# Kernel tuning notes

Hardware: AMD Instinct MI355X
Metric: run time of the kernel (lower is better)

The kernel has to match this reference:

```python
import jax, jax.numpy as jnp
import numpy as np

# dims (match init_kwargs)
N = 262144      # num_memory_locations
D = 128         # dim_memory
C = 512         # dim_controller_output
E_IN = 256      # dim_external_input
OUT = 256       # dim_NTM_output
R = 2           # num_read_heads
WH = 1          # num_write_heads
RAD = 1         # shift_radius
S = 2 * RAD + 1 # shift vector length
EPS = 1e-8


def setup_inputs() -> dict:
    key = jax.random.key(0)
    ks = jax.random.split(key, 40)
    f = lambda i, shape, s=0.05: jax.random.normal(ks[i], shape, dtype=jnp.float32) * s
    inp = {
        "external_input": f(0, (E_IN,), 1.0),
        "M": f(1, (N, D), 1.0),                      # memory matrix
        "prev_read": jnp.zeros((R, D), jnp.float32),  # first step: past readings are zeros
        "Wc": f(2, (C, E_IN + R * D)), "bc": f(3, (C,)),
        "Wo": f(4, (OUT, C + R * D)), "bo": f(5, (OUT,)),
        # read heads (stacked over head axis)
        "rWk": f(6, (R, D, C)),  "rbk": f(7, (R, D)),
        "rWb": f(8, (R, C)),     "rbb": f(9, (R,)),
        "rWg": f(10, (R, C)),    "rbg": f(11, (R,)),
        "rWs": f(12, (R, S, C)), "rbs": f(13, (R, S)),
        "rWgm": f(14, (R, C)),   "rbgm": f(15, (R,)),
        "rinit": f(16, (R, N), 1.0),
        # write heads
        "wWk": f(17, (WH, D, C)),  "wbk": f(18, (WH, D)),
        "wWb": f(19, (WH, C)),     "wbb": f(20, (WH,)),
        "wWg": f(21, (WH, C)),     "wbg": f(22, (WH,)),
        "wWs": f(23, (WH, S, C)),  "wbs": f(24, (WH, S)),
        "wWgm": f(25, (WH, C)),    "wbgm": f(26, (WH,)),
        "wWe": f(27, (WH, D, C)),  "wbe": f(28, (WH, D)),
        "wWa": f(29, (WH, D, C)),  "wba": f(30, (WH, D)),
        "winit": f(31, (WH, N), 1.0),
    }
    return inp


def _address(c, M, Mnorm, w_prev, Wk, bk, Wb, bb, Wg, bg, Ws, bs, Wgm, bgm):
    """Standard NTM addressing: content -> interpolate -> circular shift -> sharpen."""
    k = jnp.tanh(Wk @ c + bk)                       # [D] key
    beta = jax.nn.softplus(Wb @ c + bb)             # scalar key strength
    g = jax.nn.sigmoid(Wg @ c + bg)                 # scalar interpolation gate
    s = jax.nn.softmax(Ws @ c + bs)                 # [S] shift distribution
    gamma = 1.0 + jax.nn.softplus(Wgm @ c + bgm)    # scalar sharpening >= 1
    # content addressing: cosine similarity against all N memory rows
    sim = (M @ k) / (Mnorm * jnp.linalg.norm(k) + EPS)   # [N]
    w_c = jax.nn.softmax(beta * sim)
    # interpolation with previous weighting
    w_g = g * w_c + (1.0 - g) * w_prev
    # circular convolution shift (small fixed radius -> unrolled)
    w_t = jnp.zeros_like(w_g)
    for j, sh in enumerate(range(-RAD, RAD + 1)):
        w_t = w_t + s[j] * jnp.roll(w_g, sh)
    # sharpening
    w_p = w_t ** gamma
    return w_p / (w_p.sum() + EPS)


_address_heads = jax.vmap(_address, in_axes=(None, None, None, 0, 0, 0, 0, 0, 0, 0, 0, 0, 0, 0))


def reference(external_input, M, prev_read, Wc, bc, Wo, bo,
              rWk, rbk, rWb, rbb, rWg, rbg, rWs, rbs, rWgm, rbgm, rinit,
              wWk, wbk, wWb, wbb, wWg, wbg, wWs, wbs, wWgm, wbgm,
              wWe, wbe, wWa, wba, winit):
    # controller
    c = Wc @ jnp.concatenate([external_input, prev_read.reshape(-1)]) + bc   # [C]
    Mnorm = jnp.linalg.norm(M, axis=1)                                        # [N]
    # read heads: addressing (initial weighting = softmax of learned logits) then read
    w_prev_r = jax.nn.softmax(rinit, axis=1)
    read_w = _address_heads(c, M, Mnorm, w_prev_r,
                            rWk, rbk, rWb, rbb, rWg, rbg, rWs, rbs, rWgm, rbgm)  # [R, N]
    readings = read_w @ M                                                     # [R, D]
    # write heads: all weightings computed on pre-write memory
    w_prev_w = jax.nn.softmax(winit, axis=1)
    write_w = _address_heads(c, M, Mnorm, w_prev_w,
                             wWk, wbk, wWb, wbb, wWg, wbg, wWs, wbs, wWgm, wbgm)  # [WH, N]
    # sequential erase-then-add writes
    M_new = M
    for i in range(WH):
        e = jax.nn.sigmoid(wWe[i] @ c + wbe[i])   # [D] erase vector
        a = jnp.tanh(wWa[i] @ c + wba[i])          # [D] add vector
        w = write_w[i][:, None]                    # [N, 1]
        M_new = M_new * (1.0 - w * e[None, :]) + w * a[None, :]
    # NTM output
    out = Wo @ jnp.concatenate([c, readings.reshape(-1)]) + bo               # [OUT]
    return out, readings, read_w, write_w, M_new
```

## Files before the change

kernel.cpp:

```cpp
#include <hip/hip_runtime.h>
#include <hip/hip_bf16.h>

#define NN 262144
#define EPS 1e-8f

#define WS_C      0
#define WS_K      512
#define WS_E      896
#define WS_A      1024
#define WS_KNSQ   1152
#define WS_BETA   1155
#define WS_G      1158
#define WS_GAMMA  1161
#define WS_SL     1164
#define WS_ZC     1184
#define WS_SUMP   1190
#define WS_ZCR    1280
#define WS_SUMPR  1792
#define WS_RDACC  2304
#define WS_ZERO_CNT (WS_RDACC + 2048 - WS_KNSQ)
#define WS_T      4608
#define WS_NEEDED ((size_t)(WS_T + 3 * NN) * 4)

#define OUT_OUT   0
#define OUT_READ  256
#define OUT_RW    512
#define OUT_WW    (512 + 2 * NN)
#define OUT_MNEW  ((size_t)(512 + 3 * NN))

__global__ void FFNTM_78477642433000_kernel(int* p) { if (p) *p = 0; }

__device__ __forceinline__ float4 ld4(const float* p) { return *reinterpret_cast<const float4*>(p); }

__device__ __forceinline__ float wred(float v) {
#pragma unroll
    for (int off = 32; off > 0; off >>= 1) v += __shfl_xor(v, off);
    return v;
}

__device__ __forceinline__ void load_shift_params(const float* __restrict__ ws,
        float g[3], float gam[3], float izc[3], float izp[3],
        float s0[3], float s1[3], float s2[3]) {
#pragma unroll
    for (int h = 0; h < 3; h++) {
        g[h]   = ws[WS_G + h];
        gam[h] = ws[WS_GAMMA + h];
        izc[h] = 1.0f / fmaxf(ws[WS_ZC + h],     1e-30f);
        izp[h] = 1.0f / fmaxf(ws[WS_ZC + 3 + h], 1e-30f);
        const float l0 = ws[WS_SL + h*3], l1 = ws[WS_SL + h*3 + 1], l2 = ws[WS_SL + h*3 + 2];
        const float mx = fmaxf(l0, fmaxf(l1, l2));
        const float e0 = expf(l0 - mx), e1 = expf(l1 - mx), e2 = expf(l2 - mx);
        const float inv = 1.0f / (e0 + e1 + e2);
        s0[h] = e0 * inv; s1[h] = e1 * inv; s2[h] = e2 * inv;
    }
}

__global__ void csent(float* out, float val) {
    if (threadIdx.x == 0 && blockIdx.x == 0) out[OUT_OUT] = val;
}

__global__ void __launch_bounds__(256) c0(const float* __restrict__ ei, const float* __restrict__ pr,
                                          const float* __restrict__ Wc, const float* __restrict__ bc,
                                          float* __restrict__ ws) {
    const int t = threadIdx.x;
    const int lane = t & 63;
    const int j = (blockIdx.x * 256 + t) >> 6;

    if (blockIdx.x == 0) {
        for (int i = t; i < WS_ZERO_CNT; i += 256) ws[WS_KNSQ + i] = 0.0f;
    }

    const float* xs = (lane < 32) ? (ei + lane * 8) : (pr + (lane - 32) * 8);
    const float4 xa = ld4(xs), xb = ld4(xs + 4);
    const float* wr = Wc + j * 512 + lane * 8;
    const float4 wa = ld4(wr), wb = ld4(wr + 4);
    float acc = xa.x * wa.x + xa.y * wa.y + xa.z * wa.z + xa.w * wa.w
              + xb.x * wb.x + xb.y * wb.y + xb.z * wb.z + xb.w * wb.w;
    acc = wred(acc);
    if (lane == 0) ws[WS_C + j] = acc + bc[j];
}

__global__ void __launch_bounds__(256) c1(
    const float* __restrict__ rWk, const float* __restrict__ rbk,
    const float* __restrict__ rWb, const float* __restrict__ rbb,
    const float* __restrict__ rWg, const float* __restrict__ rbg,
    const float* __restrict__ rWs, const float* __restrict__ rbs,
    const float* __restrict__ rWgm, const float* __restrict__ rbgm,
    const float* __restrict__ wWk, const float* __restrict__ wbk,
    const float* __restrict__ wWb, const float* __restrict__ wbb,
    const float* __restrict__ wWg, const float* __restrict__ wbg,
    const float* __restrict__ wWs, const float* __restrict__ wbs,
    const float* __restrict__ wWgm, const float* __restrict__ wbgm,
    const float* __restrict__ wWe, const float* __restrict__ wbe,
    const float* __restrict__ wWa, const float* __restrict__ wba,
    float* __restrict__ ws) {
    const int w = blockIdx.x * 4 + (threadIdx.x >> 6);
    const int lane = threadIdx.x & 63;
    if (w >= 658) return;

    const float4 ca = ld4(ws + WS_C + lane * 8);
    const float4 cb = ld4(ws + WS_C + lane * 8 + 4);

    const float* row; float bias; int kind; int h = 0, d = 0, sidx = 0;
    if (w < 384) {
        h = w >> 7; d = w & 127;
        row  = (h < 2) ? (rWk + (h * 128 + d) * 512) : (wWk + d * 512);
        bias = (h < 2) ? rbk[h * 128 + d] : wbk[d];
        kind = 0;
    } else if (w < 512) {
        d = w - 384; row = wWe + d * 512; bias = wbe[d]; kind = 1;
    } else if (w < 640) {
        d = w - 512; row = wWa + d * 512; bias = wba[d]; kind = 2;
    } else if (w < 643) {
        h = w - 640; row = (h < 2) ? (rWb + h * 512) : wWb;
        bias = (h < 2) ? rbb[h] : wbb[0]; kind = 3;
    } else if (w < 646) {
        h = w - 643; row = (h < 2) ? (rWg + h * 512) : wWg;
        bias = (h < 2) ? rbg[h] : wbg[0]; kind = 4;
    } else if (w < 649) {
        h = w - 646; row = (h < 2) ? (rWgm + h * 512) : wWgm;
        bias = (h < 2) ? rbgm[h] : wbgm[0]; kind = 5;
    } else {
        sidx = w - 649; h = sidx / 3; const int jj = sidx % 3;
        row  = (h < 2) ? (rWs + (h * 3 + jj) * 512) : (wWs + jj * 512);
        bias = (h < 2) ? rbs[h * 3 + jj] : wbs[jj];
        kind = 6;
    }

    const float4 ra = ld4(row + lane * 8);
    const float4 rb = ld4(row + lane * 8 + 4);
    float acc = ca.x * ra.x + ca.y * ra.y + ca.z * ra.z + ca.w * ra.w
              + cb.x * rb.x + cb.y * rb.y + cb.z * rb.z + cb.w * rb.w;
    acc = wred(acc);

    if (lane == 0) {
        const float x = acc + bias;
        switch (kind) {
            case 0: { float kv = tanhf(x); ws[WS_K + w] = kv; atomicAdd(&ws[WS_KNSQ + h], kv * kv); } break;
            case 1: ws[WS_E + d] = 1.0f / (1.0f + expf(-x)); break;
            case 2: ws[WS_A + d] = tanhf(x); break;
            case 3: ws[WS_BETA + h] = log1pf(expf(x)); break;
            case 4: ws[WS_G + h] = 1.0f / (1.0f + expf(-x)); break;
            case 5: ws[WS_GAMMA + h] = 1.0f + log1pf(expf(x)); break;
            case 6: ws[WS_SL + sidx] = x; break;
        }
    }
}

__global__ void __launch_bounds__(256) c2(const float* __restrict__ M, const float* __restrict__ rinit,
                                          const float* __restrict__ winit, float* __restrict__ out,
                                          float* __restrict__ ws) {
    const int t = threadIdx.x;
    const int lane = t & 63;
    const int wv = t >> 6;
    const int grp = t >> 5;
    const int sub = lane & 31;

    float kf0[4], kf1[4], kf2[4];
#pragma unroll
    for (int j = 0; j < 4; j++) {
        kf0[j] = ws[WS_K +       sub * 4 + j];
        kf1[j] = ws[WS_K + 128 + sub * 4 + j];
        kf2[j] = ws[WS_K + 256 + sub * 4 + j];
    }
    float beta[3], kn[3];
#pragma unroll
    for (int h = 0; h < 3; h++) { kn[h] = sqrtf(ws[WS_KNSQ + h]); beta[h] = ws[WS_BETA + h]; }

    float zc0 = 0, zc1 = 0, zc2 = 0, zp0 = 0, zp1 = 0, zp2 = 0;

    for (int row = blockIdx.x * 8 + grp; row < NN; row += gridDim.x * 8) {
        const float4 m = ld4(M + (size_t)row * 128 + sub * 4);
        float d0 = m.x * kf0[0] + m.y * kf0[1] + m.z * kf0[2] + m.w * kf0[3];
        float d1 = m.x * kf1[0] + m.y * kf1[1] + m.z * kf1[2] + m.w * kf1[3];
        float d2 = m.x * kf2[0] + m.y * kf2[1] + m.z * kf2[2] + m.w * kf2[3];
        float ns = m.x * m.x + m.y * m.y + m.z * m.z + m.w * m.w;
#pragma unroll
        for (int off = 1; off < 32; off <<= 1) {
            d0 += __shfl_xor(d0, off);
            d1 += __shfl_xor(d1, off);
            d2 += __shfl_xor(d2, off);
            ns += __shfl_xor(ns, off);
        }
        if (sub == 0) {
            const float mn = sqrtf(ns);
            const float t0 = expf(beta[0] * d0 / (mn * kn[0] + EPS));
            const float t1 = expf(beta[1] * d1 / (mn * kn[1] + EPS));
            const float t2 = expf(beta[2] * d2 / (mn * kn[2] + EPS));
            ws[WS_T + row]          = t0;
            ws[WS_T + NN + row]     = t1;
            ws[WS_T + 2 * NN + row] = t2;
            zc0 += t0; zc1 += t1; zc2 += t2;
        }
    }

    float* Esc = out + OUT_MNEW;
    for (int i = blockIdx.x * 256 + t; i < NN; i += gridDim.x * 256) {
        const float e0 = expf(rinit[i]);
        const float e1 = expf(rinit[NN + i]);
        const float e2 = expf(winit[i]);
        Esc[i]          = e0;
        Esc[NN + i]     = e1;
        Esc[2 * NN + i] = e2;
        zp0 += e0; zp1 += e1; zp2 += e2;
    }

    __shared__ float red[4][6];
    float vals[6] = {zc0, zc1, zc2, zp0, zp1, zp2};
#pragma unroll
    for (int q = 0; q < 6; q++) {
        float v = wred(vals[q]);
        if (lane == 0) red[wv][q] = v;
    }
    __syncthreads();
    if (t < 6) {
        atomicAdd(&ws[WS_ZCR + (blockIdx.x & 15) * 32 + t],
                  red[0][t] + red[1][t] + red[2][t] + red[3][t]);
    }
}

__global__ void c2b(float* __restrict__ ws) {
    const int t = threadIdx.x;
    if (t < 6) {
        float s = 0.0f;
#pragma unroll
        for (int r = 0; r < 16; r++) s += ws[WS_ZCR + r * 32 + t];
        ws[WS_ZC + t] = s;
    }
}

__global__ void __launch_bounds__(256) c3(float* __restrict__ out, float* __restrict__ ws) {
    float g[3], gam[3], izc[3], izp[3], s0[3], s1[3], s2[3];
    load_shift_params(ws, g, gam, izc, izp, s0, s1, s2);
    const float* Esc = out + OUT_MNEW;

    float sump[3] = {0.f, 0.f, 0.f};
    for (int i = blockIdx.x * 256 + threadIdx.x; i < NN; i += gridDim.x * 256) {
        const int im = (i == 0) ? (NN - 1) : (i - 1);
        const int ip = (i == NN - 1) ? 0 : (i + 1);
#pragma unroll
        for (int h = 0; h < 3; h++) {
            const float* tp = ws + WS_T + h * NN;
            const float* Ep = Esc + (size_t)h * NN;
            const float gg = g[h], om = 1.0f - gg;
            const float wgm = gg * tp[im] * izc[h] + om * Ep[im] * izp[h];
            const float wg0 = gg * tp[i]  * izc[h] + om * Ep[i]  * izp[h];
            const float wgp = gg * tp[ip] * izc[h] + om * Ep[ip] * izp[h];
            const float wt = fmaxf(s0[h] * wgp + s1[h] * wg0 + s2[h] * wgm, 1e-30f);
            const float p = expf(gam[h] * logf(wt));
            sump[h] += p;
            float* pd = (h == 0) ? (out + OUT_RW) : (h == 1) ? (out + OUT_RW + NN) : (out + OUT_WW);
            pd[i] = p;
        }
    }

    __shared__ float red[4][3];
    const int lane = threadIdx.x & 63, wv = threadIdx.x >> 6;
#pragma unroll
    for (int h = 0; h < 3; h++) {
        float v = wred(sump[h]);
        if (lane == 0) red[wv][h] = v;
    }
    __syncthreads();
    if (threadIdx.x < 3) {
        atomicAdd(&ws[WS_SUMPR + (blockIdx.x & 15) * 32 + threadIdx.x],
                  red[0][threadIdx.x] + red[1][threadIdx.x] + red[2][threadIdx.x] + red[3][threadIdx.x]);
    }
}

__global__ void c3b(float* __restrict__ ws) {
    const int t = threadIdx.x;
    if (t < 3) {
        float s = 0.0f;
#pragma unroll
        for (int r = 0; r < 16; r++) s += ws[WS_SUMPR + r * 32 + t];
        ws[WS_SUMP + t] = s;
    }
}

__global__ void __launch_bounds__(256) c4(const float* __restrict__ M, float* __restrict__ out,
                                          float* __restrict__ ws) {
    float isp[3];
#pragma unroll
    for (int h = 0; h < 3; h++) isp[h] = 1.0f / (ws[WS_SUMP + h] + EPS);

    const int t = threadIdx.x;
    const int lane = t & 63;
    const int wv = t >> 6;
    const int grp = t >> 5;
    const int sub = lane & 31;

    float ev[4], av[4];
#pragma unroll
    for (int j = 0; j < 4; j++) { ev[j] = ws[WS_E + sub * 4 + j]; av[j] = ws[WS_A + sub * 4 + j]; }

    float r0[4] = {0, 0, 0, 0}, r1[4] = {0, 0, 0, 0};

    for (int row = blockIdx.x * 8 + grp; row < NN; row += gridDim.x * 8) {
        const float w0 = out[OUT_RW + row]      * isp[0];
        const float w1 = out[OUT_RW + NN + row] * isp[1];
        const float w2 = out[OUT_WW + row]      * isp[2];
        const float4 m = ld4(M + (size_t)row * 128 + sub * 4);
        float4 nv;
        nv.x = m.x * (1.0f - w2 * ev[0]) + w2 * av[0];
        nv.y = m.y * (1.0f - w2 * ev[1]) + w2 * av[1];
        nv.z = m.z * (1.0f - w2 * ev[2]) + w2 * av[2];
        nv.w = m.w * (1.0f - w2 * ev[3]) + w2 * av[3];
        *reinterpret_cast<float4*>(out + OUT_MNEW + (size_t)row * 128 + sub * 4) = nv;
        r0[0] += w0 * m.x; r0[1] += w0 * m.y; r0[2] += w0 * m.z; r0[3] += w0 * m.w;
        r1[0] += w1 * m.x; r1[1] += w1 * m.y; r1[2] += w1 * m.z; r1[3] += w1 * m.w;
        if (sub == 0) {
            out[OUT_RW + row]      = w0;
            out[OUT_RW + NN + row] = w1;
            out[OUT_WW + row]      = w2;
        }
    }

#pragma unroll
    for (int j = 0; j < 4; j++) {
        r0[j] += __shfl_xor(r0[j], 32);
        r1[j] += __shfl_xor(r1[j], 32);
    }
    __shared__ float lds[4][256];
    if (lane < 32) {
#pragma unroll
        for (int j = 0; j < 4; j++) {
            lds[wv][sub * 4 + j]       = r0[j];
            lds[wv][128 + sub * 4 + j] = r1[j];
        }
    }
    __syncthreads();
    atomicAdd(&ws[WS_RDACC + (blockIdx.x & 7) * 256 + t],
              lds[0][t] + lds[1][t] + lds[2][t] + lds[3][t]);
}

__global__ void __launch_bounds__(256) c5(const float* __restrict__ Wo, const float* __restrict__ bo,
                                          float* __restrict__ ws, float* __restrict__ out) {
    __shared__ float rd[256];
    const int t = threadIdx.x;
    {
        float s = 0.0f;
#pragma unroll
        for (int r = 0; r < 8; r++) s += ws[WS_RDACC + r * 256 + t];
        rd[t] = s;
    }
    __syncthreads();

    const int lane = t & 63;
    const int j = blockIdx.x * 4 + (t >> 6);
    const float* row = Wo + j * 768;
    float acc = 0.0f;
#pragma unroll
    for (int q = 0; q < 12; q++) {
        const int i = lane * 12 + q;
        const float x = (i < 512) ? ws[WS_C + i] : rd[i - 512];
        acc += row[i] * x;
    }
    acc = wred(acc);
    if (lane == 0) out[OUT_OUT + j] = acc + bo[j];
    if (blockIdx.x == 0) out[OUT_READ + t] = rd[t];
}

extern "C" void kernel_launch(void* const* d_in, const int* in_sizes, int n_in,
                              void* d_out, int out_size, void* d_ws, size_t ws_size,
                              hipStream_t stream) {
    float* out = (float*)d_out;

    static const int expect[33] = {
        256, 33554432, 256, 262144, 512, 196608, 256,
        131072, 256, 1024, 2, 1024, 2, 3072, 6, 1024, 2, 524288,
        65536, 128, 512, 1, 512, 1, 1536, 3, 512, 1,
        65536, 128, 65536, 128, 262144
    };
    int bad = (n_in == 33) ? -1 : 33;
    if (bad < 0) {
        for (int i = 0; i < 33; i++) {
            if (in_sizes[i] != expect[i]) { bad = i; break; }
        }
    }
    if (bad >= 0) { csent<<<1, 64, 0, stream>>>(out, 10000.0f + (float)bad); return; }
    if (ws_size < WS_NEEDED) { csent<<<1, 64, 0, stream>>>(out, 5000.0f + (float)(ws_size >> 20)); return; }

    const float* ei    = (const float*)d_in[0];
    const float* M     = (const float*)d_in[1];
    const float* pr    = (const float*)d_in[2];
    const float* Wc    = (const float*)d_in[3];
    const float* bc    = (const float*)d_in[4];
    const float* Wo    = (const float*)d_in[5];
    const float* bo    = (const float*)d_in[6];
    const float* rWk   = (const float*)d_in[7];
    const float* rbk   = (const float*)d_in[8];
    const float* rWb   = (const float*)d_in[9];
    const float* rbb   = (const float*)d_in[10];
    const float* rWg   = (const float*)d_in[11];
    const float* rbg   = (const float*)d_in[12];
    const float* rWs   = (const float*)d_in[13];
    const float* rbs   = (const float*)d_in[14];
    const float* rWgm  = (const float*)d_in[15];
    const float* rbgm  = (const float*)d_in[16];
    const float* rinit = (const float*)d_in[17];
    const float* wWk   = (const float*)d_in[18];
    const float* wbk   = (const float*)d_in[19];
    const float* wWb   = (const float*)d_in[20];
    const float* wbb   = (const float*)d_in[21];
    const float* wWg   = (const float*)d_in[22];
    const float* wbg   = (const float*)d_in[23];
    const float* wWs   = (const float*)d_in[24];
    const float* wbs   = (const float*)d_in[25];
    const float* wWgm  = (const float*)d_in[26];
    const float* wbgm  = (const float*)d_in[27];
    const float* wWe   = (const float*)d_in[28];
    const float* wbe   = (const float*)d_in[29];
    const float* wWa   = (const float*)d_in[30];
    const float* wba   = (const float*)d_in[31];
    const float* winit = (const float*)d_in[32];
    float* ws = (float*)d_ws;

    c0<<<128, 256, 0, stream>>>(ei, pr, Wc, bc, ws);
    c1<<<165, 256, 0, stream>>>(rWk, rbk, rWb, rbb, rWg, rbg, rWs, rbs, rWgm, rbgm,
                                wWk, wbk, wWb, wbb, wWg, wbg, wWs, wbs, wWgm, wbgm,
                                wWe, wbe, wWa, wba, ws);
    c2<<<2048, 256, 0, stream>>>(M, rinit, winit, out, ws);
    c2b<<<1, 64, 0, stream>>>(ws);
    c3<<<1024, 256, 0, stream>>>(out, ws);
    c3b<<<1, 64, 0, stream>>>(ws);
    c4<<<1024, 256, 0, stream>>>(M, out, ws);
    c5<<<64, 256, 0, stream>>>(Wo, bo, ws, out);
}
```

Baseline: 354.7 us.

## Drop tiny partial-sum reduction kernels and widen per-lane row chunks in c2

Removes the single-block c2b and c3b kernels. Each block of c3 and c4 now sums the 16 partial-sum slots itself, which cuts two launches and their serialization gaps. The content-similarity pass in c2 also changes from 32 lanes per row with one float4 each to 8 lanes per row with four float4 each. That shortens the shuffle reduction from five steps to three and puts 32 rows in each block. The trade-off is more registers for the key fragments, redundant tiny reductions in every block, and less coalescing per load instruction.

```diff
diff --git a/kernel.cpp b/kernel.cpp
--- a/kernel.cpp
+++ b/kernel.cpp
@@ -13,8 +13,6 @@
 #define WS_G      1158
 #define WS_GAMMA  1161
 #define WS_SL     1164
-#define WS_ZC     1184
-#define WS_SUMP   1190
 #define WS_ZCR    1280
 #define WS_SUMPR  1792
 #define WS_RDACC  2304
@@ -43,10 +41,16 @@
         float s0[3], float s1[3], float s2[3]) {
 #pragma unroll
     for (int h = 0; h < 3; h++) {
+        float zc = 0.0f, zp = 0.0f;
+#pragma unroll
+        for (int r = 0; r < 16; r++) {
+            zc += ws[WS_ZCR + r * 32 + h];
+            zp += ws[WS_ZCR + r * 32 + 3 + h];
+        }
         g[h]   = ws[WS_G + h];
         gam[h] = ws[WS_GAMMA + h];
-        izc[h] = 1.0f / fmaxf(ws[WS_ZC + h],     1e-30f);
-        izp[h] = 1.0f / fmaxf(ws[WS_ZC + 3 + h], 1e-30f);
+        izc[h] = 1.0f / fmaxf(zc, 1e-30f);
+        izp[h] = 1.0f / fmaxf(zp, 1e-30f);
         const float l0 = ws[WS_SL + h*3], l1 = ws[WS_SL + h*3 + 1], l2 = ws[WS_SL + h*3 + 2];
         const float mx = fmaxf(l0, fmaxf(l1, l2));
         const float e0 = expf(l0 - mx), e1 = expf(l1 - mx), e2 = expf(l2 - mx);
@@ -153,15 +157,15 @@
     const int t = threadIdx.x;
     const int lane = t & 63;
     const int wv = t >> 6;
-    const int grp = t >> 5;
-    const int sub = lane & 31;
-
-    float kf0[4], kf1[4], kf2[4];
-#pragma unroll
-    for (int j = 0; j < 4; j++) {
-        kf0[j] = ws[WS_K +       sub * 4 + j];
-        kf1[j] = ws[WS_K + 128 + sub * 4 + j];
-        kf2[j] = ws[WS_K + 256 + sub * 4 + j];
+    const int rl = lane >> 3;
+    const int cl = lane & 7;
+
+    float kf0[16], kf1[16], kf2[16];
+#pragma unroll
+    for (int j = 0; j < 16; j++) {
+        kf0[j] = ws[WS_K +       cl * 16 + j];
+        kf1[j] = ws[WS_K + 128 + cl * 16 + j];
+        kf2[j] = ws[WS_K + 256 + cl * 16 + j];
     }
     float beta[3], kn[3];
 #pragma unroll
@@ -169,20 +173,25 @@
 
     float zc0 = 0, zc1 = 0, zc2 = 0, zp0 = 0, zp1 = 0, zp2 = 0;
 
-    for (int row = blockIdx.x * 8 + grp; row < NN; row += gridDim.x * 8) {
-        const float4 m = ld4(M + (size_t)row * 128 + sub * 4);
-        float d0 = m.x * kf0[0] + m.y * kf0[1] + m.z * kf0[2] + m.w * kf0[3];
-        float d1 = m.x * kf1[0] + m.y * kf1[1] + m.z * kf1[2] + m.w * kf1[3];
-        float d2 = m.x * kf2[0] + m.y * kf2[1] + m.z * kf2[2] + m.w * kf2[3];
-        float ns = m.x * m.x + m.y * m.y + m.z * m.z + m.w * m.w;
-#pragma unroll
-        for (int off = 1; off < 32; off <<= 1) {
+    for (int row = blockIdx.x * 32 + wv * 8 + rl; row < NN; row += gridDim.x * 32) {
+        const float* mp = M + (size_t)row * 128 + cl * 16;
+        float d0 = 0, d1 = 0, d2 = 0, ns = 0;
+#pragma unroll
+        for (int q = 0; q < 4; q++) {
+            const float4 m = ld4(mp + q * 4);
+            d0 += m.x * kf0[q*4+0] + m.y * kf0[q*4+1] + m.z * kf0[q*4+2] + m.w * kf0[q*4+3];
+            d1 += m.x * kf1[q*4+0] + m.y * kf1[q*4+1] + m.z * kf1[q*4+2] + m.w * kf1[q*4+3];
+            d2 += m.x * kf2[q*4+0] + m.y * kf2[q*4+1] + m.z * kf2[q*4+2] + m.w * kf2[q*4+3];
+            ns += m.x * m.x + m.y * m.y + m.z * m.z + m.w * m.w;
+        }
+#pragma unroll
+        for (int off = 1; off < 8; off <<= 1) {
             d0 += __shfl_xor(d0, off);
             d1 += __shfl_xor(d1, off);
             d2 += __shfl_xor(d2, off);
             ns += __shfl_xor(ns, off);
         }
-        if (sub == 0) {
+        if (cl == 0) {
             const float mn = sqrtf(ns);
             const float t0 = expf(beta[0] * d0 / (mn * kn[0] + EPS));
             const float t1 = expf(beta[1] * d1 / (mn * kn[1] + EPS));
@@ -216,16 +225,6 @@
     if (t < 6) {
         atomicAdd(&ws[WS_ZCR + (blockIdx.x & 15) * 32 + t],
                   red[0][t] + red[1][t] + red[2][t] + red[3][t]);
-    }
-}
-
-__global__ void c2b(float* __restrict__ ws) {
-    const int t = threadIdx.x;
-    if (t < 6) {
-        float s = 0.0f;
-#pragma unroll
-        for (int r = 0; r < 16; r++) s += ws[WS_ZCR + r * 32 + t];
-        ws[WS_ZC + t] = s;
     }
 }
 
@@ -268,21 +267,16 @@
     }
 }
 
-__global__ void c3b(float* __restrict__ ws) {
-    const int t = threadIdx.x;
-    if (t < 3) {
-        float s = 0.0f;
-#pragma unroll
-        for (int r = 0; r < 16; r++) s += ws[WS_SUMPR + r * 32 + t];
-        ws[WS_SUMP + t] = s;
-    }
-}
-
 __global__ void __launch_bounds__(256) c4(const float* __restrict__ M, float* __restrict__ out,
                                           float* __restrict__ ws) {
     float isp[3];
 #pragma unroll
-    for (int h = 0; h < 3; h++) isp[h] = 1.0f / (ws[WS_SUMP + h] + EPS);
+    for (int h = 0; h < 3; h++) {
+        float s = 0.0f;
+#pragma unroll
+        for (int r = 0; r < 16; r++) s += ws[WS_SUMPR + r * 32 + h];
+        isp[h] = 1.0f / (s + EPS);
+    }
 
     const int t = threadIdx.x;
     const int lane = t & 63;
@@ -421,9 +415,7 @@
                                 wWk, wbk, wWb, wbb, wWg, wbg, wWs, wbs, wWgm, wbgm,
                                 wWe, wbe, wWa, wba, ws);
     c2<<<2048, 256, 0, stream>>>(M, rinit, winit, out, ws);
-    c2b<<<1, 64, 0, stream>>>(ws);
     c3<<<1024, 256, 0, stream>>>(out, ws);
-    c3b<<<1, 64, 0, stream>>>(ws);
     c4<<<1024, 256, 0, stream>>>(M, out, ws);
     c5<<<64, 256, 0, stream>>>(Wo, bo, ws, out);
 }
```

Measured after the change: 349.4 us. No clear change (-1.5%).
